# Performance work log

Hardware: AMD Instinct MI355X
Metric: run time of the kernel (lower is better)

## Reference

```python
import jax, jax.numpy as jnp
import numpy as np

B, IN, H, O, L, G = 4096, 512, 1024, 256, 2, 3


def _lin_init(key, out_dim, in_dim):
    k1, k2 = jax.random.split(key)
    bound = 1.0 / np.sqrt(in_dim)
    w = jax.random.uniform(k1, (out_dim, in_dim), jnp.float32, -bound, bound)
    b = jax.random.uniform(k2, (out_dim,), jnp.float32, -bound, bound)
    return w, b


def setup_inputs() -> dict:
    key = jax.random.key(0)
    ks = jax.random.split(key, 10)
    x = jax.random.normal(ks[0], (B, IN), jnp.float32)
    hidden = jax.random.normal(ks[1], (L, B, H), jnp.float32)
    i2d_w, i2d_b = _lin_init(ks[2], H, IN)
    # stacked GRU params, PyTorch gate order (r, z, n); layer0 input dim == H (after i2d)
    kih = jax.random.split(ks[3], L)
    khh = jax.random.split(ks[4], L)
    gru_w_ih = jnp.stack([_lin_init(kih[l], 3 * H, H)[0] for l in range(L)])
    gru_b_ih = jnp.stack([_lin_init(kih[l], 3 * H, H)[1] for l in range(L)])
    gru_w_hh = jnp.stack([_lin_init(khh[l], 3 * H, H)[0] for l in range(L)])
    gru_b_hh = jnp.stack([_lin_init(khh[l], 3 * H, H)[1] for l in range(L)])
    mu_w, mu_b = _lin_init(ks[5], O * G, H)
    sigma_w, sigma_b = _lin_init(ks[6], O * G, H)
    pi_w, pi_b = _lin_init(ks[7], O * G, H)
    return {"x": x, "hidden": hidden, "i2d_w": i2d_w, "i2d_b": i2d_b,
            "gru_w_ih": gru_w_ih, "gru_w_hh": gru_w_hh,
            "gru_b_ih": gru_b_ih, "gru_b_hh": gru_b_hh,
            "mu_w": mu_w, "mu_b": mu_b, "sigma_w": sigma_w, "sigma_b": sigma_b,
            "pi_w": pi_w, "pi_b": pi_b, "batch_size": B}


def reference(x, hidden, i2d_w, i2d_b, gru_w_ih, gru_w_hh, gru_b_ih, gru_b_hh,
              mu_w, mu_b, sigma_w, sigma_b, pi_w, pi_b, batch_size):
    # input projection + relu
    h1 = jax.nn.relu(x @ i2d_w.T + i2d_b)  # [B, H]
    # single-timestep stacked GRU (PyTorch cell math, gate order r,z,n)
    inp = h1
    new_h = []
    for l in range(hidden.shape[0]):
        h_prev = hidden[l]
        gi = inp @ gru_w_ih[l].T + gru_b_ih[l]   # [B, 3H]
        gh = h_prev @ gru_w_hh[l].T + gru_b_hh[l]
        i_r, i_z, i_n = jnp.split(gi, 3, axis=-1)
        h_r, h_z, h_n = jnp.split(gh, 3, axis=-1)
        r = jax.nn.sigmoid(i_r + h_r)
        z = jax.nn.sigmoid(i_z + h_z)
        n = jnp.tanh(i_n + r * h_n)
        h_new = (1.0 - z) * n + z * h_prev
        new_h.append(h_new)
        inp = h_new
    hidden_out = jnp.stack(new_h)            # [L, B, H]
    h_out = jnp.tanh(inp)                    # [B, H]
    n_g = 3
    o = mu_w.shape[0] // n_g
    pi = jax.nn.softmax((h_out @ pi_w.T + pi_b).reshape(-1, n_g, o), axis=1)
    mu = (h_out @ mu_w.T + mu_b).reshape(-1, n_g, o)
    sig = jax.nn.softplus(h_out @ sigma_w.T + sigma_b).reshape(-1, n_g, o)
    return (mu, sig, pi, hidden_out)
```

## Files before the change

kernel.cpp:

```cpp
#include <hip/hip_runtime.h>
#include <stdint.h>

typedef unsigned short bf16u;
typedef float f32x4 __attribute__((ext_vector_type(4)));
typedef short bf16x8 __attribute__((ext_vector_type(8)));
typedef float f4 __attribute__((ext_vector_type(4)));

__device__ __forceinline__ float b2f(bf16u u) {
  union { uint32_t i; float f; } v; v.i = ((uint32_t)u) << 16; return v.f;
}
__device__ __forceinline__ uint32_t f2b(float f) {
  union { float f; uint32_t i; } v; v.f = f;
  uint32_t i = v.i;
  return (i + 0x7FFFu + ((i >> 16) & 1u)) >> 16;
}
__device__ __forceinline__ float sigm(float x) { return 1.f / (1.f + __expf(-x)); }

struct CvtSeg { const float* src; char* dst; int blk0; int count; int tobf16; };
struct CvtArgs { CvtSeg s[12]; int nseg; };

__global__ __launch_bounds__(256)
void cvt_multi(CvtArgs a) {
  int b = blockIdx.x, seg = 0;
  while (seg + 1 < a.nseg && b >= a.s[seg + 1].blk0) ++seg;
  const CvtSeg& S = a.s[seg];
  size_t idx = ((size_t)(b - S.blk0) * 2048) + (size_t)threadIdx.x * 8;
  if ((long long)idx >= S.count) return;
  f4 x = *(const f4*)&S.src[idx];
  f4 y = *(const f4*)&S.src[idx + 4];
  if (S.tobf16) {
    uint4 o;
    o.x = (f2b(x[0]) & 0xffffu) | (f2b(x[1]) << 16);
    o.y = (f2b(x[2]) & 0xffffu) | (f2b(x[3]) << 16);
    o.z = (f2b(y[0]) & 0xffffu) | (f2b(y[1]) << 16);
    o.w = (f2b(y[2]) & 0xffffu) | (f2b(y[3]) << 16);
    *(uint4*)((bf16u*)S.dst + idx) = o;
  } else {
    *(f4*)((float*)S.dst + idx) = x;
    *(f4*)((float*)S.dst + idx + 4) = y;
  }
}

struct GemmPtrs {
  const bf16u* A[2];
  const bf16u* W[2];
  const float* bias[2];
  void* C[2];
};

template <int IT, int ACT, int OUTF32>
__global__ __launch_bounds__(256)
void gemm_bt(GemmPtrs p, int N, int K) {
  constexpr int BM = IT * 32;
  __shared__ bf16u sA[BM * 64];
  __shared__ bf16u sB[128 * 64];
  const int z = blockIdx.z;
  const bf16u* __restrict__ A = p.A[z];
  const bf16u* __restrict__ W = p.W[z];
  const float* __restrict__ bias = p.bias[z];

  const int tid  = threadIdx.x;
  const int wave = tid >> 6;
  const int lane = tid & 63;
  const int bn = blockIdx.x, bm = blockIdx.y;

  const int srA = wave * (IT * 8) + (lane >> 3);
  const int srB = wave * 32 + (lane >> 3);
  const int kc  = (lane & 7) ^ ((lane >> 3) & 7);
  const bf16u* ag = A + (size_t)(bm * BM + srA) * K + kc * 8;
  const bf16u* wg = W + (size_t)(bn * 128 + srB) * K + kc * 8;

  const int wm = wave >> 1, wn = wave & 1;
  const int q = lane >> 4, cl = lane & 15;

  int aoff[IT][2], boff[4][2];
#pragma unroll
  for (int i = 0; i < IT; ++i) {
    int m = wm * (IT * 16) + i * 16 + cl;
#pragma unroll
    for (int kk = 0; kk < 2; ++kk)
      aoff[i][kk] = m * 64 + (((q + kk * 4) ^ (m & 7)) * 8);
  }
#pragma unroll
  for (int j = 0; j < 4; ++j) {
    int n = wn * 64 + j * 16 + cl;
#pragma unroll
    for (int kk = 0; kk < 2; ++kk)
      boff[j][kk] = n * 64 + (((q + kk * 4) ^ (n & 7)) * 8);
  }

  f32x4 acc[IT][4] = {};

  for (int k0 = 0; k0 < K; k0 += 64) {
#pragma unroll
    for (int t = 0; t < IT; ++t)
      __builtin_amdgcn_global_load_lds(
          (const __attribute__((address_space(1))) void*)(ag + k0 + (size_t)t * 8 * K),
          (__attribute__((address_space(3))) void*)&sA[wave * IT * 512 + t * 512],
          16, 0, 0);
#pragma unroll
    for (int t = 0; t < 4; ++t)
      __builtin_amdgcn_global_load_lds(
          (const __attribute__((address_space(1))) void*)(wg + k0 + (size_t)t * 8 * K),
          (__attribute__((address_space(3))) void*)&sB[wave * 2048 + t * 512],
          16, 0, 0);
    __syncthreads();
#pragma unroll
    for (int kk = 0; kk < 2; ++kk) {
      bf16x8 af[IT], bfr[4];
#pragma unroll
      for (int i = 0; i < IT; ++i) af[i] = *(const bf16x8*)&sA[aoff[i][kk]];
#pragma unroll
      for (int j = 0; j < 4; ++j) bfr[j] = *(const bf16x8*)&sB[boff[j][kk]];
#pragma unroll
      for (int i = 0; i < IT; ++i)
#pragma unroll
        for (int j = 0; j < 4; ++j)
          acc[i][j] = __builtin_amdgcn_mfma_f32_16x16x32_bf16(af[i], bfr[j], acc[i][j], 0, 0, 0);
    }
    __syncthreads();
  }

  float bv[4];
#pragma unroll
  for (int j = 0; j < 4; ++j)
    bv[j] = bias[bn * 128 + wn * 64 + j * 16 + cl];

  const int row0 = bm * BM + wm * (IT * 16) + q * 4;
  const int col0 = bn * 128 + wn * 64 + cl;
#pragma unroll
  for (int i = 0; i < IT; ++i)
#pragma unroll
    for (int j = 0; j < 4; ++j)
#pragma unroll
      for (int r = 0; r < 4; ++r) {
        float v = acc[i][j][r] + bv[j];
        if (ACT == 1) v = fmaxf(v, 0.f);
        size_t off = (size_t)(row0 + i * 16 + r) * N + (col0 + j * 16);
        if (OUTF32) ((float*)p.C[z])[off] = v;
        else        ((bf16u*)p.C[z])[off] = (bf16u)f2b(v);
      }
}

__global__ __launch_bounds__(256)
void gemm_heads(const bf16u* __restrict__ A, const bf16u* __restrict__ Wp,
                const float* __restrict__ biasp, float* __restrict__ out_mu,
                float* __restrict__ out_sg, float* __restrict__ rawpi,
                int outHS) {
  constexpr int K = 1024;
  __shared__ bf16u sA[64 * 64];
  __shared__ bf16u sB[128 * 64];
  const int tid  = threadIdx.x;
  const int wave = tid >> 6;
  const int lane = tid & 63;
  const int bn = blockIdx.x, bm = blockIdx.y;

  const int srA = wave * 16 + (lane >> 3);
  const int srB = wave * 32 + (lane >> 3);
  const int kc  = (lane & 7) ^ ((lane >> 3) & 7);
  const bf16u* ag = A + (size_t)(bm * 64 + srA) * K + kc * 8;
  const bf16u* wg = Wp + (size_t)(bn * 128 + srB) * K + kc * 8;

  const int wm = wave >> 1, wn = wave & 1;
  const int q = lane >> 4, cl = lane & 15;

  int aoff[2][2], boff[4][2];
#pragma unroll
  for (int i = 0; i < 2; ++i) {
    int m = wm * 32 + i * 16 + cl;
#pragma unroll
    for (int kk = 0; kk < 2; ++kk)
      aoff[i][kk] = m * 64 + (((q + kk * 4) ^ (m & 7)) * 8);
  }
#pragma unroll
  for (int j = 0; j < 4; ++j) {
    int n = wn * 64 + j * 16 + cl;
#pragma unroll
    for (int kk = 0; kk < 2; ++kk)
      boff[j][kk] = n * 64 + (((q + kk * 4) ^ (n & 7)) * 8);
  }

  f32x4 acc[2][4] = {};
  for (int k0 = 0; k0 < K; k0 += 64) {
#pragma unroll
    for (int t = 0; t < 2; ++t)
      __builtin_amdgcn_global_load_lds(
          (const __attribute__((address_space(1))) void*)(ag + k0 + (size_t)t * 8 * K),
          (__attribute__((address_space(3))) void*)&sA[wave * 1024 + t * 512],
          16, 0, 0);
#pragma unroll
    for (int t = 0; t < 4; ++t)
      __builtin_amdgcn_global_load_lds(
          (const __attribute__((address_space(1))) void*)(wg + k0 + (size_t)t * 8 * K),
          (__attribute__((address_space(3))) void*)&sB[wave * 2048 + t * 512],
          16, 0, 0);
    __syncthreads();
#pragma unroll
    for (int kk = 0; kk < 2; ++kk) {
      bf16x8 af[2], bfr[4];
#pragma unroll
      for (int i = 0; i < 2; ++i) af[i] = *(const bf16x8*)&sA[aoff[i][kk]];
#pragma unroll
      for (int j = 0; j < 4; ++j) bfr[j] = *(const bf16x8*)&sB[boff[j][kk]];
#pragma unroll
      for (int i = 0; i < 2; ++i)
#pragma unroll
        for (int j = 0; j < 4; ++j)
          acc[i][j] = __builtin_amdgcn_mfma_f32_16x16x32_bf16(af[i], bfr[j], acc[i][j], 0, 0, 0);
    }
    __syncthreads();
  }

  float bv[4];
#pragma unroll
  for (int j = 0; j < 4; ++j)
    bv[j] = biasp[bn * 128 + wn * 64 + j * 16 + cl];

  const int head = bn / 6;
  const int ch0 = (bn % 6) * 128 + wn * 64 + cl;
  const int row0 = bm * 64 + wm * 32 + q * 4;
#pragma unroll
  for (int i = 0; i < 2; ++i)
#pragma unroll
    for (int j = 0; j < 4; ++j)
#pragma unroll
      for (int r = 0; r < 4; ++r) {
        float v = acc[i][j][r] + bv[j];
        size_t off = (size_t)(row0 + i * 16 + r) * 768 + (ch0 + j * 16);
        if (head == 0) out_mu[off] = v;
        else if (head == 1)
          out_sg[(size_t)0 + off] = fmaxf(v, 0.f) + log1pf(__expf(-fabsf(v)));
        else rawpi[off] = v;
      }
}

struct __align__(16) V8 { uint32_t u[4]; };
__device__ __forceinline__ float getf(const V8& v, int k) {
  uint32_t w = v.u[k >> 1];
  return b2f((bf16u)((k & 1) ? (w >> 16) : (w & 0xffffu)));
}
__device__ __forceinline__ void setb(V8& v, int k, float f) {
  uint32_t b = f2b(f) & 0xffffu;
  if (k & 1) v.u[k >> 1] = (v.u[k >> 1] & 0x0000ffffu) | (b << 16);
  else       v.u[k >> 1] = (v.u[k >> 1] & 0xffff0000u) | b;
}

template <int LAST>
__global__ __launch_bounds__(256)
void gru_gates(const bf16u* __restrict__ gi, const bf16u* __restrict__ gh,
               const float* __restrict__ hprev, float* __restrict__ hid_out,
               bf16u* __restrict__ nxt) {
  int t = blockIdx.x * 256 + threadIdx.x;
  size_t idx = (size_t)t * 8;
  int b = (int)(idx >> 10);
  int h = (int)(idx & 1023);
  size_t g0 = (size_t)b * 3072 + h;
  V8 ir  = *(const V8*)&gi[g0];
  V8 izv = *(const V8*)&gi[g0 + 1024];
  V8 inv = *(const V8*)&gi[g0 + 2048];
  V8 hr  = *(const V8*)&gh[g0];
  V8 hzv = *(const V8*)&gh[g0 + 1024];
  V8 hnv = *(const V8*)&gh[g0 + 2048];
  f4 hp0 = *(const f4*)&hprev[idx];
  f4 hp1 = *(const f4*)&hprev[idx + 4];
  f4 o0, o1;
  V8 no = {};
#pragma unroll
  for (int k = 0; k < 8; ++k) {
    float hpv = (k < 4) ? hp0[k] : hp1[k - 4];
    float r  = sigm(getf(ir, k) + getf(hr, k));
    float zg = sigm(getf(izv, k) + getf(hzv, k));
    float n  = tanhf(getf(inv, k) + r * getf(hnv, k));
    float hnew = (1.f - zg) * n + zg * hpv;
    if (k < 4) o0[k] = hnew; else o1[k - 4] = hnew;
    setb(no, k, LAST ? tanhf(hnew) : hnew);
  }
  *(f4*)&hid_out[idx] = o0;
  *(f4*)&hid_out[idx + 4] = o1;
  *(V8*)&nxt[idx] = no;
}

__global__ __launch_bounds__(256)
void pi_softmax(const float* __restrict__ rawpi, float* __restrict__ out) {
  int t = blockIdx.x * 256 + threadIdx.x;
  int b = t >> 6;
  int o4 = (t & 63) << 2;
  size_t rb = (size_t)b * 768 + o4;
  f4 pi0 = *(const f4*)&rawpi[rb];
  f4 pi1 = *(const f4*)&rawpi[rb + 256];
  f4 pi2 = *(const f4*)&rawpi[rb + 512];
  f4 e0v, e1v, e2v;
#pragma unroll
  for (int c = 0; c < 4; ++c) {
    float m = fmaxf(fmaxf(pi0[c], pi1[c]), pi2[c]);
    float e0 = __expf(pi0[c] - m), e1 = __expf(pi1[c] - m), e2 = __expf(pi2[c] - m);
    float s = 1.f / (e0 + e1 + e2);
    e0v[c] = e0 * s; e1v[c] = e1 * s; e2v[c] = e2 * s;
  }
  *(f4*)&out[rb]       = e0v;
  *(f4*)&out[rb + 256] = e1v;
  *(f4*)&out[rb + 512] = e2v;
}

extern "C" void kernel_launch(void* const* d_in, const int* in_sizes, int n_in,
                              void* d_out, int out_size, void* d_ws, size_t ws_size,
                              hipStream_t stream) {
  const float* x      = (const float*)d_in[0];
  const float* hidden = (const float*)d_in[1];
  const float* i2d_w  = (const float*)d_in[2];
  const float* i2d_b  = (const float*)d_in[3];
  const float* w_ih   = (const float*)d_in[4];
  const float* w_hh   = (const float*)d_in[5];
  const float* b_ih   = (const float*)d_in[6];
  const float* b_hh   = (const float*)d_in[7];
  const float* mu_w   = (const float*)d_in[8];
  const float* mu_b   = (const float*)d_in[9];
  const float* sg_w   = (const float*)d_in[10];
  const float* sg_b   = (const float*)d_in[11];
  const float* pi_w   = (const float*)d_in[12];
  const float* pi_b   = (const float*)d_in[13];
  float* out = (float*)d_out;

  const size_t BH = 4194304;
  const int HS = 3145728;
  float* hid_base = out + (size_t)3 * HS;

  dim3 blk(256, 1, 1);

  bf16u* wb_i2d = (bf16u*)d_ws;
  bf16u* wb_ih  = wb_i2d + 524288;
  bf16u* wb_hh  = wb_ih + 6291456;
  bf16u* wb_hd  = wb_hh + 6291456;
  float* biasp  = (float*)((char*)d_ws + 30932992);
  const size_t wbytes = 30942208;

  {
    CvtArgs a{};
    int nb = 0;
    auto seg = [&](const float* s, void* d, int count, int tobf) {
      a.s[a.nseg++] = {s, (char*)d, nb, count, tobf};
      nb += (count + 2047) / 2048;
    };
    seg(i2d_w, wb_i2d, 524288, 1);
    seg(w_ih,  wb_ih, 6291456, 1);
    seg(w_hh,  wb_hh, 6291456, 1);
    seg(mu_w,  wb_hd, 786432, 1);
    seg(sg_w,  wb_hd + 786432, 786432, 1);
    seg(pi_w,  wb_hd + 1572864, 786432, 1);
    seg(mu_b,  biasp, 768, 0);
    seg(sg_b,  biasp + 768, 768, 0);
    seg(pi_b,  biasp + 1536, 768, 0);
    cvt_multi<<<dim3(nb), blk, 0, stream>>>(a);
  }

  int Bc = 4096;
  while (wbytes + (size_t)Bc * 19456 > ws_size && Bc > 256) Bc >>= 1;
  const int nchunk = 4096 / Bc;

  char* cbase = (char*)d_ws + wbytes;
  bf16u* ws0 = (bf16u*)cbase;
  bf16u* xb  = (bf16u*)(cbase + (size_t)Bc * 2048);
  bf16u* hb0 = (bf16u*)(cbase + (size_t)Bc * 3072);
  bf16u* hb1 = (bf16u*)(cbase + (size_t)Bc * 5120);
  bf16u* gi  = (bf16u*)(cbase + (size_t)Bc * 7168);
  bf16u* gh  = (bf16u*)(cbase + (size_t)Bc * 13312);
  float* rawpi = (float*)gi;

  for (int c = 0; c < nchunk; ++c) {
    const size_t off = (size_t)c * Bc;
    const float* h0_c = hidden + off * 1024;
    const float* h1_c = hidden + BH + off * 1024;

    {
      CvtArgs a{};
      int nb = 0;
      auto seg = [&](const float* s, void* d, int count) {
        a.s[a.nseg++] = {s, (char*)d, nb, count, 1};
        nb += (count + 2047) / 2048;
      };
      seg(x + off * 512, xb, Bc * 512);
      seg(h0_c, hb0, Bc * 1024);
      seg(h1_c, hb1, Bc * 1024);
      cvt_multi<<<dim3(nb), blk, 0, stream>>>(a);
    }

    {
      GemmPtrs p{};
      p.A[0] = xb; p.W[0] = wb_i2d; p.bias[0] = i2d_b; p.C[0] = ws0;
      gemm_bt<2, 1, 0><<<dim3(8, Bc / 64, 1), blk, 0, stream>>>(p, 1024, 512);
    }
    {
      GemmPtrs p{};
      p.A[0] = ws0; p.W[0] = wb_ih; p.bias[0] = b_ih; p.C[0] = gi;
      p.A[1] = hb0; p.W[1] = wb_hh; p.bias[1] = b_hh; p.C[1] = gh;
      gemm_bt<4, 0, 0><<<dim3(24, Bc / 128, 2), blk, 0, stream>>>(p, 3072, 1024);
    }
    gru_gates<0><<<dim3(Bc / 2), blk, 0, stream>>>(
        gi, gh, h0_c, hid_base + off * 1024, ws0);
    {
      GemmPtrs p{};
      p.A[0] = ws0; p.W[0] = wb_ih + 3145728; p.bias[0] = b_ih + 3072; p.C[0] = gi;
      p.A[1] = hb1; p.W[1] = wb_hh + 3145728; p.bias[1] = b_hh + 3072; p.C[1] = gh;
      gemm_bt<4, 0, 0><<<dim3(24, Bc / 128, 2), blk, 0, stream>>>(p, 3072, 1024);
    }
    gru_gates<1><<<dim3(Bc / 2), blk, 0, stream>>>(
        gi, gh, h1_c, hid_base + BH + off * 1024, ws0);
    gemm_heads<<<dim3(18, Bc / 64, 1), blk, 0, stream>>>(
        ws0, wb_hd, biasp, out + off * 768, out + HS + off * 768, rawpi, HS);
    pi_softmax<<<dim3(Bc / 4), blk, 0, stream>>>(rawpi, out + 2 * (size_t)HS + off * 768);
  }
}
```

Measured before the change: 389.6 us.

## Add 256x128-tile triple-buffered gate GEMM with direct global-to-LDS loads

Adds a dedicated GEMM kernel for the GRU gate projections. It uses 512-thread blocks with 256x128 output tiles, a three-stage LDS ring filled by global_load_lds, XOR-swizzled LDS layout, and raised priority around the MFMA blocks. The intent is to get more reuse per loaded tile and to overlap memory loads with MFMA work in the dominant GEMMs. In exchange the tile is larger, which means fewer blocks (24x16x2) and about 144KB of LDS per block, so occupancy may be limited.

Measured after the change: 412.2 us. 1.06x slower.

```diff
diff --git a/kernel.cpp b/kernel.cpp
--- a/kernel.cpp
+++ b/kernel.cpp
@@ -139,6 +139,114 @@
         size_t off = (size_t)(row0 + i * 16 + r) * N + (col0 + j * 16);
         if (OUTF32) ((float*)p.C[z])[off] = v;
         else        ((bf16u*)p.C[z])[off] = (bf16u)f2b(v);
+      }
+}
+
+__global__ __launch_bounds__(512, 2)
+void gemm_gates(GemmPtrs p, int N, int K) {
+  __shared__ bf16u sA[3][256 * 64];
+  __shared__ bf16u sB[3][128 * 64];
+  const int z = blockIdx.z;
+  const bf16u* __restrict__ A = p.A[z];
+  const bf16u* __restrict__ W = p.W[z];
+  const float* __restrict__ bias = p.bias[z];
+
+  const int tid  = threadIdx.x;
+  const int wave = tid >> 6;
+  const int lane = tid & 63;
+  const int bn = blockIdx.x, bm = blockIdx.y;
+
+  const int rr = tid >> 3;
+  const int kc = (tid & 7) ^ (rr & 7);
+  const bf16u* ag = A + (size_t)(bm * 256 + rr) * K + kc * 8;
+  const bf16u* wg = W + (size_t)(bn * 128 + rr) * K + kc * 8;
+
+  const int wm = wave >> 1, wn = wave & 1;
+  const int q = lane >> 4, cl = lane & 15;
+
+  int aoff[4][2], boff[4][2];
+#pragma unroll
+  for (int i = 0; i < 4; ++i) {
+    int m = wm * 64 + i * 16 + cl;
+#pragma unroll
+    for (int kk = 0; kk < 2; ++kk)
+      aoff[i][kk] = m * 64 + (((q + kk * 4) ^ (m & 7)) * 8);
+  }
+#pragma unroll
+  for (int j = 0; j < 4; ++j) {
+    int n = wn * 64 + j * 16 + cl;
+#pragma unroll
+    for (int kk = 0; kk < 2; ++kk)
+      boff[j][kk] = n * 64 + (((q + kk * 4) ^ (n & 7)) * 8);
+  }
+
+  f32x4 acc[4][4] = {};
+  const int NT = K >> 6;
+
+#define STAGE_G(buf, t)                                                          \
+  do {                                                                           \
+    _Pragma("unroll")                                                            \
+    for (int s = 0; s < 4; ++s)                                                  \
+      __builtin_amdgcn_global_load_lds(                                          \
+          (const __attribute__((address_space(1))) void*)(ag + (size_t)(t) * 64 + (size_t)(s * 64) * K), \
+          (__attribute__((address_space(3))) void*)&sA[buf][(s * 64 + wave * 8) * 64], 16, 0, 0);        \
+    _Pragma("unroll")                                                            \
+    for (int s = 0; s < 2; ++s)                                                  \
+      __builtin_amdgcn_global_load_lds(                                          \
+          (const __attribute__((address_space(1))) void*)(wg + (size_t)(t) * 64 + (size_t)(s * 64) * K), \
+          (__attribute__((address_space(3))) void*)&sB[buf][(s * 64 + wave * 8) * 64], 16, 0, 0);        \
+  } while (0)
+
+  STAGE_G(0, 0);
+  STAGE_G(1, 1);
+
+  int c = 0;
+  for (int kt = 0; kt < NT; ++kt) {
+    if (kt + 1 < NT) asm volatile("s_waitcnt vmcnt(6)" ::: "memory");
+    else             asm volatile("s_waitcnt vmcnt(0)" ::: "memory");
+    __builtin_amdgcn_s_barrier();
+    asm volatile("" ::: "memory");
+    if (kt + 2 < NT) {
+      const int sb = (c == 0) ? 2 : c - 1;
+      STAGE_G(sb, kt + 2);
+    }
+    bf16x8 af[4][2], bfr[4][2];
+#pragma unroll
+    for (int kk = 0; kk < 2; ++kk) {
+#pragma unroll
+      for (int i = 0; i < 4; ++i) af[i][kk] = *(const bf16x8*)&sA[c][aoff[i][kk]];
+#pragma unroll
+      for (int j = 0; j < 4; ++j) bfr[j][kk] = *(const bf16x8*)&sB[c][boff[j][kk]];
+    }
+    __builtin_amdgcn_s_setprio(1);
+#pragma unroll
+    for (int kk = 0; kk < 2; ++kk)
+#pragma unroll
+      for (int i = 0; i < 4; ++i)
+#pragma unroll
+        for (int j = 0; j < 4; ++j)
+          acc[i][j] = __builtin_amdgcn_mfma_f32_16x16x32_bf16(af[i][kk], bfr[j][kk], acc[i][j], 0, 0, 0);
+    __builtin_amdgcn_s_setprio(0);
+    c = (c == 2) ? 0 : c + 1;
+  }
+#undef STAGE_G
+
+  float bv[4];
+#pragma unroll
+  for (int j = 0; j < 4; ++j)
+    bv[j] = bias[bn * 128 + wn * 64 + j * 16 + cl];
+
+  const int row0 = bm * 256 + wm * 64 + q * 4;
+  const int col0 = bn * 128 + wn * 64 + cl;
+#pragma unroll
+  for (int i = 0; i < 4; ++i)
+#pragma unroll
+    for (int j = 0; j < 4; ++j)
+#pragma unroll
+      for (int r = 0; r < 4; ++r) {
+        float v = acc[i][j][r] + bv[j];
+        size_t off = (size_t)(row0 + i * 16 + r) * N + (col0 + j * 16);
+        ((bf16u*)p.C[z])[off] = (bf16u)f2b(v);
       }
 }
 
@@ -393,7 +501,7 @@
       GemmPtrs p{};
       p.A[0] = ws0; p.W[0] = wb_ih; p.bias[0] = b_ih; p.C[0] = gi;
       p.A[1] = hb0; p.W[1] = wb_hh; p.bias[1] = b_hh; p.C[1] = gh;
-      gemm_bt<4, 0, 0><<<dim3(24, Bc / 128, 2), blk, 0, stream>>>(p, 3072, 1024);
+      gemm_gates<<<dim3(24, Bc / 256, 2), dim3(512, 1, 1), 0, stream>>>(p, 3072, 1024);
     }
     gru_gates<0><<<dim3(Bc / 2), blk, 0, stream>>>(
         gi, gh, h0_c, hid_base + off * 1024, ws0);
@@ -401,7 +509,7 @@
       GemmPtrs p{};
       p.A[0] = ws0; p.W[0] = wb_ih + 3145728; p.bias[0] = b_ih + 3072; p.C[0] = gi;
       p.A[1] = hb1; p.W[1] = wb_hh + 3145728; p.bias[1] = b_hh + 3072; p.C[1] = gh;
-      gemm_bt<4, 0, 0><<<dim3(24, Bc / 128, 2), blk, 0, stream>>>(p, 3072, 1024);
+      gemm_gates<<<dim3(24, Bc / 256, 2), dim3(512, 1, 1), 0, stream>>>(p, 3072, 1024);
     }
     gru_gates<1><<<dim3(Bc / 2), blk, 0, stream>>>(
         gi, gh, h1_c, hid_base + BH + off * 1024, ws0);
```

## Add 256x256 multi-buffered pipelined GEMM for GRU gate projections; use fast tanh

Applied to the files above, without the earlier changes.

Adds a new GEMM kernel for the GRU gate projections. It uses 512-thread blocks with 256x256 tiles, four LDS buffers with loads issued three tiles ahead via global_load_lds, explicit vmcnt waits, barrier-split MFMA phases and s_setprio. The goal is to raise data reuse and hide global-memory latency, which the older single-buffered 128-row kernel did not. The gate kernel also replaces tanhf with an exp-based approximation to cut transcendental cost. The larger tiles produce fewer blocks, which may reduce occupancy, and the exp-based tanh can lose accuracy or overflow to inf for large inputs.

Result: slower. 418.8 us (+7.5%).

```diff
diff --git a/kernel.cpp b/kernel.cpp
--- a/kernel.cpp
+++ b/kernel.cpp
@@ -6,6 +6,9 @@
 typedef short bf16x8 __attribute__((ext_vector_type(8)));
 typedef float f4 __attribute__((ext_vector_type(4)));
 
+#define AS1 __attribute__((address_space(1)))
+#define AS3 __attribute__((address_space(3)))
+
 __device__ __forceinline__ float b2f(bf16u u) {
   union { uint32_t i; float f; } v; v.i = ((uint32_t)u) << 16; return v.f;
 }
@@ -15,6 +18,10 @@
   return (i + 0x7FFFu + ((i >> 16) & 1u)) >> 16;
 }
 __device__ __forceinline__ float sigm(float x) { return 1.f / (1.f + __expf(-x)); }
+__device__ __forceinline__ float ftanh(float x) {
+  float e = __expf(2.f * x);
+  return 1.f - 2.f / (e + 1.f);
+}
 
 struct CvtSeg { const float* src; char* dst; int blk0; int count; int tobf16; };
 struct CvtArgs { CvtSeg s[12]; int nseg; };
@@ -95,14 +102,14 @@
 #pragma unroll
     for (int t = 0; t < IT; ++t)
       __builtin_amdgcn_global_load_lds(
-          (const __attribute__((address_space(1))) void*)(ag + k0 + (size_t)t * 8 * K),
-          (__attribute__((address_space(3))) void*)&sA[wave * IT * 512 + t * 512],
+          (const AS1 void*)(ag + k0 + (size_t)t * 8 * K),
+          (AS3 void*)&sA[wave * IT * 512 + t * 512],
           16, 0, 0);
 #pragma unroll
     for (int t = 0; t < 4; ++t)
       __builtin_amdgcn_global_load_lds(
-          (const __attribute__((address_space(1))) void*)(wg + k0 + (size_t)t * 8 * K),
-          (__attribute__((address_space(3))) void*)&sB[wave * 2048 + t * 512],
+          (const AS1 void*)(wg + k0 + (size_t)t * 8 * K),
+          (AS3 void*)&sB[wave * 2048 + t * 512],
           16, 0, 0);
     __syncthreads();
 #pragma unroll
@@ -139,6 +146,132 @@
         size_t off = (size_t)(row0 + i * 16 + r) * N + (col0 + j * 16);
         if (OUTF32) ((float*)p.C[z])[off] = v;
         else        ((bf16u*)p.C[z])[off] = (bf16u)f2b(v);
+      }
+}
+
+__global__ __launch_bounds__(512, 2)
+void gemm_gates8(GemmPtrs p, int N, int K) {
+  __shared__ bf16u sA[4][256 * 32];
+  __shared__ bf16u sB[4][256 * 32];
+  const int z = blockIdx.z;
+  const bf16u* __restrict__ A = p.A[z];
+  const bf16u* __restrict__ W = p.W[z];
+  const float* __restrict__ bias = p.bias[z];
+
+  const int tid  = threadIdx.x;
+  const int wave = tid >> 6;
+  const int lane = tid & 63;
+  const int bn = blockIdx.x, bm = blockIdx.y;
+
+  const int rg0 = wave * 8 + (lane >> 3);
+  const int sp  = (lane & 7) ^ (rg0 & 7);
+  const int srow = rg0 * 2 + (sp >> 2);
+  const int sch  = sp & 3;
+  const bf16u* agA = A + (size_t)(bm * 256 + srow) * K + sch * 8;
+  const bf16u* wgB = W + (size_t)(bn * 256 + srow) * K + sch * 8;
+  const int ldsoff = wave * 512;
+
+  const int wm = wave >> 2, wn = wave & 3;
+  const int q = lane >> 4, cl = lane & 15;
+
+  int aoff[8], boff[4];
+#pragma unroll
+  for (int m = 0; m < 8; ++m) {
+    int row = wm * 128 + m * 16 + cl;
+    aoff[m] = (row >> 1) * 64 + (((((row & 1) << 2) | q) ^ ((row >> 1) & 7)) * 8);
+  }
+#pragma unroll
+  for (int j = 0; j < 4; ++j) {
+    int row = wn * 64 + j * 16 + cl;
+    boff[j] = (row >> 1) * 64 + (((((row & 1) << 2) | q) ^ ((row >> 1) & 7)) * 8);
+  }
+
+  f32x4 acc[8][4] = {};
+  const int NT = K >> 5;
+
+#define STG_A(buf, t)                                                         \
+  do {                                                                        \
+    __builtin_amdgcn_global_load_lds((const AS1 void*)(agA + (t) * 32),       \
+        (AS3 void*)&sA[buf][ldsoff], 16, 0, 0);                               \
+    __builtin_amdgcn_global_load_lds((const AS1 void*)(agA + (t) * 32 + (size_t)128 * K), \
+        (AS3 void*)&sA[buf][ldsoff + 4096], 16, 0, 0);                        \
+  } while (0)
+#define STG_B(buf, t)                                                         \
+  do {                                                                        \
+    __builtin_amdgcn_global_load_lds((const AS1 void*)(wgB + (t) * 32),       \
+        (AS3 void*)&sB[buf][ldsoff], 16, 0, 0);                               \
+    __builtin_amdgcn_global_load_lds((const AS1 void*)(wgB + (t) * 32 + (size_t)128 * K), \
+        (AS3 void*)&sB[buf][ldsoff + 4096], 16, 0, 0);                        \
+  } while (0)
+
+  STG_A(0, 0); STG_B(0, 0);
+  STG_A(1, 1); STG_B(1, 1);
+  STG_A(2, 2); STG_B(2, 2);
+  asm volatile("s_waitcnt vmcnt(8)" ::: "memory");
+  __builtin_amdgcn_s_barrier();
+  asm volatile("" ::: "memory");
+
+  for (int t = 0; t < NT; ++t) {
+    const int cb = t & 3;
+    const int pb = (t + 3) & 3;
+    const bool st = (t + 3) < NT;
+    bf16x8 af[8], b0, b1;
+#pragma unroll
+    for (int m = 0; m < 8; ++m) af[m] = *(const bf16x8*)&sA[cb][aoff[m]];
+    b0 = *(const bf16x8*)&sB[cb][boff[0]];
+    b1 = *(const bf16x8*)&sB[cb][boff[1]];
+    if (st) STG_A(pb, t + 3);
+    __builtin_amdgcn_s_barrier();
+    asm volatile("" ::: "memory");
+    __builtin_amdgcn_s_setprio(1);
+#pragma unroll
+    for (int m = 0; m < 8; ++m) {
+      acc[m][0] = __builtin_amdgcn_mfma_f32_16x16x32_bf16(af[m], b0, acc[m][0], 0, 0, 0);
+      acc[m][1] = __builtin_amdgcn_mfma_f32_16x16x32_bf16(af[m], b1, acc[m][1], 0, 0, 0);
+    }
+    __builtin_amdgcn_s_setprio(0);
+    __builtin_amdgcn_s_barrier();
+    asm volatile("" ::: "memory");
+    b0 = *(const bf16x8*)&sB[cb][boff[2]];
+    b1 = *(const bf16x8*)&sB[cb][boff[3]];
+    if (st) STG_B(pb, t + 3);
+    {
+      int nif = NT - 1 - t; if (nif > 3) nif = 3;
+      if (nif >= 3)      asm volatile("s_waitcnt vmcnt(8)" ::: "memory");
+      else if (nif == 2) asm volatile("s_waitcnt vmcnt(4)" ::: "memory");
+      else if (nif == 1) asm volatile("s_waitcnt vmcnt(0)" ::: "memory");
+    }
+    __builtin_amdgcn_s_barrier();
+    asm volatile("" ::: "memory");
+    __builtin_amdgcn_s_setprio(1);
+#pragma unroll
+    for (int m = 0; m < 8; ++m) {
+      acc[m][2] = __builtin_amdgcn_mfma_f32_16x16x32_bf16(af[m], b0, acc[m][2], 0, 0, 0);
+      acc[m][3] = __builtin_amdgcn_mfma_f32_16x16x32_bf16(af[m], b1, acc[m][3], 0, 0, 0);
+    }
+    __builtin_amdgcn_s_setprio(0);
+    __builtin_amdgcn_s_barrier();
+    asm volatile("" ::: "memory");
+  }
+#undef STG_A
+#undef STG_B
+
+  float bv[4];
+#pragma unroll
+  for (int j = 0; j < 4; ++j)
+    bv[j] = bias[bn * 256 + wn * 64 + j * 16 + cl];
+
+  const int row0 = bm * 256 + wm * 128 + q * 4;
+  const int col0 = bn * 256 + wn * 64 + cl;
+#pragma unroll
+  for (int m = 0; m < 8; ++m)
+#pragma unroll
+    for (int j = 0; j < 4; ++j)
+#pragma unroll
+      for (int r = 0; r < 4; ++r) {
+        float v = acc[m][j][r] + bv[j];
+        size_t off = (size_t)(row0 + m * 16 + r) * N + (col0 + j * 16);
+        ((bf16u*)p.C[z])[off] = (bf16u)f2b(v);
       }
 }
 
@@ -185,14 +318,14 @@
 #pragma unroll
     for (int t = 0; t < 2; ++t)
       __builtin_amdgcn_global_load_lds(
-          (const __attribute__((address_space(1))) void*)(ag + k0 + (size_t)t * 8 * K),
-          (__attribute__((address_space(3))) void*)&sA[wave * 1024 + t * 512],
+          (const AS1 void*)(ag + k0 + (size_t)t * 8 * K),
+          (AS3 void*)&sA[wave * 1024 + t * 512],
           16, 0, 0);
 #pragma unroll
     for (int t = 0; t < 4; ++t)
       __builtin_amdgcn_global_load_lds(
-          (const __attribute__((address_space(1))) void*)(wg + k0 + (size_t)t * 8 * K),
-          (__attribute__((address_space(3))) void*)&sB[wave * 2048 + t * 512],
+          (const AS1 void*)(wg + k0 + (size_t)t * 8 * K),
+          (AS3 void*)&sB[wave * 2048 + t * 512],
           16, 0, 0);
     __syncthreads();
 #pragma unroll
@@ -270,10 +403,10 @@
     float hpv = (k < 4) ? hp0[k] : hp1[k - 4];
     float r  = sigm(getf(ir, k) + getf(hr, k));
     float zg = sigm(getf(izv, k) + getf(hzv, k));
-    float n  = tanhf(getf(inv, k) + r * getf(hnv, k));
+    float n  = ftanh(getf(inv, k) + r * getf(hnv, k));
     float hnew = (1.f - zg) * n + zg * hpv;
     if (k < 4) o0[k] = hnew; else o1[k - 4] = hnew;
-    setb(no, k, LAST ? tanhf(hnew) : hnew);
+    setb(no, k, LAST ? ftanh(hnew) : hnew);
   }
   *(f4*)&hid_out[idx] = o0;
   *(f4*)&hid_out[idx + 4] = o1;
@@ -393,7 +526,7 @@
       GemmPtrs p{};
       p.A[0] = ws0; p.W[0] = wb_ih; p.bias[0] = b_ih; p.C[0] = gi;
       p.A[1] = hb0; p.W[1] = wb_hh; p.bias[1] = b_hh; p.C[1] = gh;
-      gemm_bt<4, 0, 0><<<dim3(24, Bc / 128, 2), blk, 0, stream>>>(p, 3072, 1024);
+      gemm_gates8<<<dim3(12, Bc / 256, 2), dim3(512, 1, 1), 0, stream>>>(p, 3072, 1024);
     }
     gru_gates<0><<<dim3(Bc / 2), blk, 0, stream>>>(
         gi, gh, h0_c, hid_base + off * 1024, ws0);
@@ -401,7 +534,7 @@
       GemmPtrs p{};
       p.A[0] = ws0; p.W[0] = wb_ih + 3145728; p.bias[0] = b_ih + 3072; p.C[0] = gi;
       p.A[1] = hb1; p.W[1] = wb_hh + 3145728; p.bias[1] = b_hh + 3072; p.C[1] = gh;
-      gemm_bt<4, 0, 0><<<dim3(24, Bc / 128, 2), blk, 0, stream>>>(p, 3072, 1024);
+      gemm_gates8<<<dim3(12, Bc / 256, 2), dim3(512, 1, 1), 0, stream>>>(p, 3072, 1024);
     }
     gru_gates<1><<<dim3(Bc / 2), blk, 0, stream>>>(
         gi, gh, h1_c, hid_base + BH + off * 1024, ws0);
```

## Fuse GRU input/hidden GEMMs with gate epilogue into a single kernel

Applied to the files above, without the earlier changes.

Replaces the per-layer pair of batched gi/gh GEMMs plus a separate elementwise gate kernel with one kernel per layer. Each block computes all six gate tiles (r,z,n for input and hidden) for a 128x64 output tile and applies the GRU cell in registers. This removes the bf16 gi/gh intermediates (write and reread of 6x B x H per layer) and two launches, and shrinks workspace. The cost is heavier blocks (512 threads, 80KB LDS, 24 accumulator tiles per wave) with lower occupancy, a smaller N tile that reloads activations more often, and scalar strided epilogue stores. Fast-math tanh and log are also swapped in.

After: 368.0 us. 5.6% less time.

```diff
diff --git a/kernel.cpp b/kernel.cpp
--- a/kernel.cpp
+++ b/kernel.cpp
@@ -6,6 +6,9 @@
 typedef short bf16x8 __attribute__((ext_vector_type(8)));
 typedef float f4 __attribute__((ext_vector_type(4)));
 
+#define AS1 __attribute__((address_space(1)))
+#define AS3 __attribute__((address_space(3)))
+
 __device__ __forceinline__ float b2f(bf16u u) {
   union { uint32_t i; float f; } v; v.i = ((uint32_t)u) << 16; return v.f;
 }
@@ -15,6 +18,10 @@
   return (i + 0x7FFFu + ((i >> 16) & 1u)) >> 16;
 }
 __device__ __forceinline__ float sigm(float x) { return 1.f / (1.f + __expf(-x)); }
+__device__ __forceinline__ float ftanh(float x) {
+  float e = __expf(2.f * x);
+  return 1.f - 2.f / (e + 1.f);
+}
 
 struct CvtSeg { const float* src; char* dst; int blk0; int count; int tobf16; };
 struct CvtArgs { CvtSeg s[12]; int nseg; };
@@ -95,14 +102,14 @@
 #pragma unroll
     for (int t = 0; t < IT; ++t)
       __builtin_amdgcn_global_load_lds(
-          (const __attribute__((address_space(1))) void*)(ag + k0 + (size_t)t * 8 * K),
-          (__attribute__((address_space(3))) void*)&sA[wave * IT * 512 + t * 512],
+          (const AS1 void*)(ag + k0 + (size_t)t * 8 * K),
+          (AS3 void*)&sA[wave * IT * 512 + t * 512],
           16, 0, 0);
 #pragma unroll
     for (int t = 0; t < 4; ++t)
       __builtin_amdgcn_global_load_lds(
-          (const __attribute__((address_space(1))) void*)(wg + k0 + (size_t)t * 8 * K),
-          (__attribute__((address_space(3))) void*)&sB[wave * 2048 + t * 512],
+          (const AS1 void*)(wg + k0 + (size_t)t * 8 * K),
+          (AS3 void*)&sB[wave * 2048 + t * 512],
           16, 0, 0);
     __syncthreads();
 #pragma unroll
@@ -139,6 +146,130 @@
         size_t off = (size_t)(row0 + i * 16 + r) * N + (col0 + j * 16);
         if (OUTF32) ((float*)p.C[z])[off] = v;
         else        ((bf16u*)p.C[z])[off] = (bf16u)f2b(v);
+      }
+}
+
+template <int LAST>
+__global__ __launch_bounds__(512)
+void gru_fused(const bf16u* __restrict__ inp, const bf16u* __restrict__ hpb,
+               const bf16u* __restrict__ wih, const bf16u* __restrict__ whh,
+               const float* __restrict__ bih, const float* __restrict__ bhh,
+               const float* __restrict__ hpf, float* __restrict__ hid_out,
+               bf16u* __restrict__ nxt) {
+  constexpr int K = 1024;
+  __shared__ bf16u s[640 * 64];
+  const int tid  = threadIdx.x;
+  const int wave = tid >> 6;
+  const int lane = tid & 63;
+  const int bn = blockIdx.x, bm = blockIdx.y;
+  const int c0 = bn * 64;
+
+  const int rr  = tid >> 3;
+  const int kc  = (tid & 7) ^ (rr & 7);
+  const int dst0 = rr * 64 + (tid & 7) * 8;
+  const bf16u* gI = inp + (size_t)(bm * 128 + rr) * K + kc * 8;
+  const bf16u* gH = hpb + (size_t)(bm * 128 + rr) * K + kc * 8;
+  const bf16u* gW[6];
+#pragma unroll
+  for (int p = 0; p < 6; ++p) {
+    const bf16u* base = (p < 3) ? wih : whh;
+    gW[p] = base + (size_t)((p % 3) * 1024 + c0 + rr) * K + kc * 8;
+  }
+
+  const int wm = wave >> 1, wn = wave & 1;
+  const int q = lane >> 4, cl = lane & 15;
+
+  int aoff[2][2], boff[2][2];
+#pragma unroll
+  for (int i = 0; i < 2; ++i) {
+    int ai = wm * 32 + i * 16 + cl;
+#pragma unroll
+    for (int kk = 0; kk < 2; ++kk)
+      aoff[i][kk] = ai * 64 + (((q + kk * 4) ^ (ai & 7)) * 8);
+  }
+#pragma unroll
+  for (int j = 0; j < 2; ++j) {
+    int br = wn * 32 + j * 16 + cl;
+#pragma unroll
+    for (int kk = 0; kk < 2; ++kk)
+      boff[j][kk] = (256 + br) * 64 + (((q + kk * 4) ^ (br & 7)) * 8);
+  }
+
+  f32x4 acc[6][2][2] = {};
+
+  for (int k0 = 0; k0 < K; k0 += 64) {
+    __builtin_amdgcn_global_load_lds((const AS1 void*)(gI + k0),
+        (AS3 void*)&s[dst0], 16, 0, 0);
+    __builtin_amdgcn_global_load_lds((const AS1 void*)(gI + k0 + (size_t)64 * K),
+        (AS3 void*)&s[dst0 + 4096], 16, 0, 0);
+    __builtin_amdgcn_global_load_lds((const AS1 void*)(gH + k0),
+        (AS3 void*)&s[dst0 + 8192], 16, 0, 0);
+    __builtin_amdgcn_global_load_lds((const AS1 void*)(gH + k0 + (size_t)64 * K),
+        (AS3 void*)&s[dst0 + 12288], 16, 0, 0);
+#pragma unroll
+    for (int p = 0; p < 6; ++p)
+      __builtin_amdgcn_global_load_lds((const AS1 void*)(gW[p] + k0),
+          (AS3 void*)&s[dst0 + (4 + p) * 4096], 16, 0, 0);
+    __syncthreads();
+#pragma unroll
+    for (int kk = 0; kk < 2; ++kk) {
+      bf16x8 aI[2], aH[2];
+#pragma unroll
+      for (int i = 0; i < 2; ++i) {
+        aI[i] = *(const bf16x8*)&s[aoff[i][kk]];
+        aH[i] = *(const bf16x8*)&s[aoff[i][kk] + 8192];
+      }
+#pragma unroll
+      for (int p = 0; p < 6; ++p) {
+        bf16x8 b0 = *(const bf16x8*)&s[boff[0][kk] + p * 4096];
+        bf16x8 b1 = *(const bf16x8*)&s[boff[1][kk] + p * 4096];
+        if (p < 3) {
+          acc[p][0][0] = __builtin_amdgcn_mfma_f32_16x16x32_bf16(aI[0], b0, acc[p][0][0], 0, 0, 0);
+          acc[p][0][1] = __builtin_amdgcn_mfma_f32_16x16x32_bf16(aI[0], b1, acc[p][0][1], 0, 0, 0);
+          acc[p][1][0] = __builtin_amdgcn_mfma_f32_16x16x32_bf16(aI[1], b0, acc[p][1][0], 0, 0, 0);
+          acc[p][1][1] = __builtin_amdgcn_mfma_f32_16x16x32_bf16(aI[1], b1, acc[p][1][1], 0, 0, 0);
+        } else {
+          acc[p][0][0] = __builtin_amdgcn_mfma_f32_16x16x32_bf16(aH[0], b0, acc[p][0][0], 0, 0, 0);
+          acc[p][0][1] = __builtin_amdgcn_mfma_f32_16x16x32_bf16(aH[0], b1, acc[p][0][1], 0, 0, 0);
+          acc[p][1][0] = __builtin_amdgcn_mfma_f32_16x16x32_bf16(aH[1], b0, acc[p][1][0], 0, 0, 0);
+          acc[p][1][1] = __builtin_amdgcn_mfma_f32_16x16x32_bf16(aH[1], b1, acc[p][1][1], 0, 0, 0);
+        }
+      }
+    }
+    __syncthreads();
+  }
+
+  float bI[3][2], bH[3][2];
+#pragma unroll
+  for (int g = 0; g < 3; ++g)
+#pragma unroll
+    for (int j = 0; j < 2; ++j) {
+      int col = c0 + wn * 32 + j * 16 + cl;
+      bI[g][j] = bih[g * 1024 + col];
+      bH[g][j] = bhh[g * 1024 + col];
+    }
+
+#pragma unroll
+  for (int i = 0; i < 2; ++i)
+#pragma unroll
+    for (int j = 0; j < 2; ++j)
+#pragma unroll
+      for (int r_ = 0; r_ < 4; ++r_) {
+        int row = bm * 128 + wm * 32 + i * 16 + q * 4 + r_;
+        int col = c0 + wn * 32 + j * 16 + cl;
+        size_t o = (size_t)row * 1024 + col;
+        float vir = acc[0][i][j][r_] + bI[0][j];
+        float viz = acc[1][i][j][r_] + bI[1][j];
+        float vin = acc[2][i][j][r_] + bI[2][j];
+        float vhr = acc[3][i][j][r_] + bH[0][j];
+        float vhz = acc[4][i][j][r_] + bH[1][j];
+        float vhn = acc[5][i][j][r_] + bH[2][j];
+        float rg = sigm(vir + vhr);
+        float zg = sigm(viz + vhz);
+        float ng = ftanh(vin + rg * vhn);
+        float hnew = (1.f - zg) * ng + zg * hpf[o];
+        hid_out[o] = hnew;
+        nxt[o] = (bf16u)f2b(LAST ? ftanh(hnew) : hnew);
       }
 }
 
@@ -185,14 +316,14 @@
 #pragma unroll
     for (int t = 0; t < 2; ++t)
       __builtin_amdgcn_global_load_lds(
-          (const __attribute__((address_space(1))) void*)(ag + k0 + (size_t)t * 8 * K),
-          (__attribute__((address_space(3))) void*)&sA[wave * 1024 + t * 512],
+          (const AS1 void*)(ag + k0 + (size_t)t * 8 * K),
+          (AS3 void*)&sA[wave * 1024 + t * 512],
           16, 0, 0);
 #pragma unroll
     for (int t = 0; t < 4; ++t)
       __builtin_amdgcn_global_load_lds(
-          (const __attribute__((address_space(1))) void*)(wg + k0 + (size_t)t * 8 * K),
-          (__attribute__((address_space(3))) void*)&sB[wave * 2048 + t * 512],
+          (const AS1 void*)(wg + k0 + (size_t)t * 8 * K),
+          (AS3 void*)&sB[wave * 2048 + t * 512],
           16, 0, 0);
     __syncthreads();
 #pragma unroll
@@ -229,55 +360,9 @@
         size_t off = (size_t)(row0 + i * 16 + r) * 768 + (ch0 + j * 16);
         if (head == 0) out_mu[off] = v;
         else if (head == 1)
-          out_sg[(size_t)0 + off] = fmaxf(v, 0.f) + log1pf(__expf(-fabsf(v)));
+          out_sg[off] = fmaxf(v, 0.f) + __logf(1.f + __expf(-fabsf(v)));
         else rawpi[off] = v;
       }
-}
-
-struct __align__(16) V8 { uint32_t u[4]; };
-__device__ __forceinline__ float getf(const V8& v, int k) {
-  uint32_t w = v.u[k >> 1];
-  return b2f((bf16u)((k & 1) ? (w >> 16) : (w & 0xffffu)));
-}
-__device__ __forceinline__ void setb(V8& v, int k, float f) {
-  uint32_t b = f2b(f) & 0xffffu;
-  if (k & 1) v.u[k >> 1] = (v.u[k >> 1] & 0x0000ffffu) | (b << 16);
-  else       v.u[k >> 1] = (v.u[k >> 1] & 0xffff0000u) | b;
-}
-
-template <int LAST>
-__global__ __launch_bounds__(256)
-void gru_gates(const bf16u* __restrict__ gi, const bf16u* __restrict__ gh,
-               const float* __restrict__ hprev, float* __restrict__ hid_out,
-               bf16u* __restrict__ nxt) {
-  int t = blockIdx.x * 256 + threadIdx.x;
-  size_t idx = (size_t)t * 8;
-  int b = (int)(idx >> 10);
-  int h = (int)(idx & 1023);
-  size_t g0 = (size_t)b * 3072 + h;
-  V8 ir  = *(const V8*)&gi[g0];
-  V8 izv = *(const V8*)&gi[g0 + 1024];
-  V8 inv = *(const V8*)&gi[g0 + 2048];
-  V8 hr  = *(const V8*)&gh[g0];
-  V8 hzv = *(const V8*)&gh[g0 + 1024];
-  V8 hnv = *(const V8*)&gh[g0 + 2048];
-  f4 hp0 = *(const f4*)&hprev[idx];
-  f4 hp1 = *(const f4*)&hprev[idx + 4];
-  f4 o0, o1;
-  V8 no = {};
-#pragma unroll
-  for (int k = 0; k < 8; ++k) {
-    float hpv = (k < 4) ? hp0[k] : hp1[k - 4];
-    float r  = sigm(getf(ir, k) + getf(hr, k));
-    float zg = sigm(getf(izv, k) + getf(hzv, k));
-    float n  = tanhf(getf(inv, k) + r * getf(hnv, k));
-    float hnew = (1.f - zg) * n + zg * hpv;
-    if (k < 4) o0[k] = hnew; else o1[k - 4] = hnew;
-    setb(no, k, LAST ? tanhf(hnew) : hnew);
-  }
-  *(f4*)&hid_out[idx] = o0;
-  *(f4*)&hid_out[idx + 4] = o1;
-  *(V8*)&nxt[idx] = no;
 }
 
 __global__ __launch_bounds__(256)
@@ -354,17 +439,16 @@
   }
 
   int Bc = 4096;
-  while (wbytes + (size_t)Bc * 19456 > ws_size && Bc > 256) Bc >>= 1;
+  while (wbytes + (size_t)Bc * 12288 > ws_size && Bc > 256) Bc >>= 1;
   const int nchunk = 4096 / Bc;
 
   char* cbase = (char*)d_ws + wbytes;
-  bf16u* ws0 = (bf16u*)cbase;
-  bf16u* xb  = (bf16u*)(cbase + (size_t)Bc * 2048);
-  bf16u* hb0 = (bf16u*)(cbase + (size_t)Bc * 3072);
-  bf16u* hb1 = (bf16u*)(cbase + (size_t)Bc * 5120);
-  bf16u* gi  = (bf16u*)(cbase + (size_t)Bc * 7168);
-  bf16u* gh  = (bf16u*)(cbase + (size_t)Bc * 13312);
-  float* rawpi = (float*)gi;
+  bf16u* ws0  = (bf16u*)cbase;
+  bf16u* xb   = (bf16u*)(cbase + (size_t)Bc * 2048);
+  bf16u* hb0  = (bf16u*)(cbase + (size_t)Bc * 3072);
+  bf16u* hb1  = (bf16u*)(cbase + (size_t)Bc * 5120);
+  bf16u* nxt0 = (bf16u*)(cbase + (size_t)Bc * 7168);
+  float* rawpi = (float*)(cbase + (size_t)Bc * 9216);
 
   for (int c = 0; c < nchunk; ++c) {
     const size_t off = (size_t)c * Bc;
@@ -389,22 +473,12 @@
       p.A[0] = xb; p.W[0] = wb_i2d; p.bias[0] = i2d_b; p.C[0] = ws0;
       gemm_bt<2, 1, 0><<<dim3(8, Bc / 64, 1), blk, 0, stream>>>(p, 1024, 512);
     }
-    {
-      GemmPtrs p{};
-      p.A[0] = ws0; p.W[0] = wb_ih; p.bias[0] = b_ih; p.C[0] = gi;
-      p.A[1] = hb0; p.W[1] = wb_hh; p.bias[1] = b_hh; p.C[1] = gh;
-      gemm_bt<4, 0, 0><<<dim3(24, Bc / 128, 2), blk, 0, stream>>>(p, 3072, 1024);
-    }
-    gru_gates<0><<<dim3(Bc / 2), blk, 0, stream>>>(
-        gi, gh, h0_c, hid_base + off * 1024, ws0);
-    {
-      GemmPtrs p{};
-      p.A[0] = ws0; p.W[0] = wb_ih + 3145728; p.bias[0] = b_ih + 3072; p.C[0] = gi;
-      p.A[1] = hb1; p.W[1] = wb_hh + 3145728; p.bias[1] = b_hh + 3072; p.C[1] = gh;
-      gemm_bt<4, 0, 0><<<dim3(24, Bc / 128, 2), blk, 0, stream>>>(p, 3072, 1024);
-    }
-    gru_gates<1><<<dim3(Bc / 2), blk, 0, stream>>>(
-        gi, gh, h1_c, hid_base + BH + off * 1024, ws0);
+    gru_fused<0><<<dim3(16, Bc / 128), dim3(512, 1, 1), 0, stream>>>(
+        ws0, hb0, wb_ih, wb_hh, b_ih, b_hh, h0_c,
+        hid_base + off * 1024, nxt0);
+    gru_fused<1><<<dim3(16, Bc / 128), dim3(512, 1, 1), 0, stream>>>(
+        nxt0, hb1, wb_ih + 3145728, wb_hh + 3145728, b_ih + 3072, b_hh + 3072,
+        h1_c, hid_base + BH + off * 1024, ws0);
     gemm_heads<<<dim3(18, Bc / 64, 1), blk, 0, stream>>>(
         ws0, wb_hd, biasp, out + off * 768, out + HS + off * 768, rawpi, HS);
     pi_softmax<<<dim3(Bc / 4), blk, 0, stream>>>(rawpi, out + 2 * (size_t)HS + off * 768);
```
